# Performance work log

Hardware: AMD Instinct MI355X
Metric: run time of the kernel (lower is better)

Reference implementation:

```python
import jax, jax.numpy as jnp
import numpy as np

N = 4096
E = 262144
IN_DIM = 256
EDGE_DIM = 16
NUM_ATOM_FEATURES = 16
LATENT_DIM = 128
NUM_BOND_TYPES = 5


def setup_inputs() -> dict:
    key = jax.random.key(0)
    ks = jax.random.split(key, 12)
    inp = {
        's': jax.random.normal(ks[0], (N, IN_DIM), dtype=jnp.float32),
        'e': jax.random.normal(ks[1], (E, EDGE_DIM), dtype=jnp.float32),
        'batch': jnp.zeros((N,), dtype=jnp.int64),
        'edge_index_global': jax.random.randint(ks[2], (2, E), 0, N, dtype=jnp.int64),
        # learned parameters (torch nn.Linear layout: W is [out, in])
        'W_shared': jax.random.normal(ks[3], (IN_DIM, IN_DIM), dtype=jnp.float32) * 0.02,
        'b_shared': jnp.zeros((IN_DIM,), dtype=jnp.float32),
        'W_bond': jax.random.normal(ks[4], (IN_DIM, EDGE_DIM), dtype=jnp.float32) * 0.02,
        'b_bond': jnp.zeros((IN_DIM,), dtype=jnp.float32),
        'W_bonds': jax.random.normal(ks[5], (NUM_BOND_TYPES, IN_DIM), dtype=jnp.float32) * 0.02,
        'b_bonds': jnp.zeros((NUM_BOND_TYPES,), dtype=jnp.float32),
        'W_atoms': jax.random.normal(ks[6], (NUM_ATOM_FEATURES + LATENT_DIM, IN_DIM), dtype=jnp.float32) * 0.02,
        'b_atoms': jnp.zeros((NUM_ATOM_FEATURES + LATENT_DIM,), dtype=jnp.float32),
    }
    return inp


def reference(s, e, batch, edge_index_global,
              W_shared, b_shared, W_bond, b_bond,
              W_bonds, b_bonds, W_atoms, b_atoms):
    # shared_mapping: Linear + SiLU
    s = jax.nn.silu(s @ W_shared.T + b_shared)  # [n, in_dim]
    j = edge_index_global[0]
    i = edge_index_global[1]
    n = s.shape[0]

    # atoms_lin then split into atom-type logits and latent prediction
    atoms_out = s @ W_atoms.T + b_atoms  # [n, num_atom_features + latent_dim]
    atoms_pred = atoms_out[:, :NUM_ATOM_FEATURES]
    latent_pred = atoms_out[:, NUM_ATOM_FEATURES:]

    # dense scatter -> symmetrize -> gather (faithful to the original O(n^2) path)
    e_dense = jnp.zeros((n, n, e.shape[-1]), dtype=e.dtype).at[j, i].set(e)
    e_dense = 0.5 * (e_dense + e_dense.transpose(1, 0, 2))
    e_sym = e_dense[j, i]  # [E, edge_dim]

    # fused gather + bond linear + SiLU + bonds linear
    f = jax.nn.silu(s[i] + s[j] + e_sym @ W_bond.T + b_bond)  # [E, in_dim]
    bonds_pred = f @ W_bonds.T + b_bonds  # [E, num_bond_types]

    return (latent_pred, atoms_pred, bonds_pred)
```

## Files before the change

### kernel.cpp

```cpp
#include <hip/hip_runtime.h>
#include <hip/hip_bf16.h>

#define N_NODES   4096
#define E_EDGES   262144
#define IN_DIM    256
#define EDGE_DIM  16
#define NAF       16
#define LATENT    128
#define NBT       5

#define LATENT_OFF 0
#define ATOMS_OFF  (N_NODES * LATENT)
#define BONDS_OFF  (ATOMS_OFF + N_NODES * NAF)

#define TBITS 20
#define TSIZE (1u << TBITS)
#define TMASK (TSIZE - 1u)

typedef float    f32x4  __attribute__((ext_vector_type(4)));
typedef float    f32x4v __attribute__((ext_vector_type(4)));
typedef short    bf16x8 __attribute__((ext_vector_type(8)));
typedef unsigned u32x2  __attribute__((ext_vector_type(2)));
typedef unsigned u32x4  __attribute__((ext_vector_type(4)));

__device__ __forceinline__ float silu_f(float x) {
    return x / (1.0f + __expf(-x));
}

__device__ __forceinline__ unsigned pack_bf16x2(float lo, float hi) {
#if __has_builtin(__builtin_amdgcn_cvt_pk_bf16_f32)
    typedef __bf16 bf16x2_t __attribute__((ext_vector_type(2)));
    union { bf16x2_t v; unsigned u; } c;
    c.v = __builtin_amdgcn_cvt_pk_bf16_f32(lo, hi);
    return c.u;
#else
    union { float f; unsigned u; } a, b;
    a.f = lo; b.f = hi;
    const unsigned ra = (a.u + 0x7FFFu + ((a.u >> 16) & 1u)) >> 16;
    const unsigned rb = (b.u + 0x7FFFu + ((b.u >> 16) & 1u)) >> 16;
    return ra | (rb << 16);
#endif
}

__device__ __forceinline__ float bf_lo(unsigned u) {
    union { unsigned x; float f; } c; c.x = u << 16; return c.f;
}
__device__ __forceinline__ float bf_hi(unsigned u) {
    union { unsigned x; float f; } c; c.x = u & 0xFFFF0000u; return c.f;
}

__device__ __forceinline__ void split_bf16(const float4 x0, const float4 x1,
                                           bf16x8* hi, bf16x8* lo) {
    union { bf16x8 v; unsigned u[4]; } H, L;
    H.u[0] = pack_bf16x2(x0.x, x0.y);
    H.u[1] = pack_bf16x2(x0.z, x0.w);
    H.u[2] = pack_bf16x2(x1.x, x1.y);
    H.u[3] = pack_bf16x2(x1.z, x1.w);
    L.u[0] = pack_bf16x2(x0.x - bf_lo(H.u[0]), x0.y - bf_hi(H.u[0]));
    L.u[1] = pack_bf16x2(x0.z - bf_lo(H.u[1]), x0.w - bf_hi(H.u[1]));
    L.u[2] = pack_bf16x2(x1.x - bf_lo(H.u[2]), x1.y - bf_hi(H.u[2]));
    L.u[3] = pack_bf16x2(x1.z - bf_lo(H.u[3]), x1.w - bf_hi(H.u[3]));
    *hi = H.v; *lo = L.v;
}

__device__ __forceinline__ void gld_lds16(const void* g, void* l) {
    __builtin_amdgcn_global_load_lds(
        (const __attribute__((address_space(1))) unsigned*)g,
        (__attribute__((address_space(3))) unsigned*)l, 16, 0, 0);
}

__device__ __forceinline__ int hlookup(const unsigned long long* __restrict__ tab,
                                       unsigned key) {
    unsigned h = (key * 2654435761u) >> (32 - TBITS);
    while (true) {
        const unsigned long long cur = tab[h];
        if (cur == 0ULL) return -1;
        if ((unsigned)(cur >> 18) == key + 1u) return (int)(cur & 0x3FFFFu);
        h = (h + 1u) & TMASK;
    }
}

__global__ __launch_bounds__(256) void k_gemm1(const float* __restrict__ s,
                                               const float* __restrict__ Wsh,
                                               const float* __restrict__ bsh,
                                               const int* __restrict__ eidx,
                                               const float* __restrict__ Wb,
                                               const float* __restrict__ bb,
                                               const float* __restrict__ Wbs,
                                               unsigned short* __restrict__ sact16,
                                               unsigned long long* __restrict__ tab,
                                               u32x4* __restrict__ A1pre,
                                               u32x4* __restrict__ A2pre) {
    const int blk = blockIdx.x;
    const int c   = threadIdx.x;

    if (blk >= 1024) {
        if (blk < 2048) {
            const int k = (blk - 1024) * 256 + c;
            const unsigned j = (unsigned)eidx[k];
            const unsigned i = (unsigned)eidx[E_EDGES + k];
            const unsigned key = (j << 12) | i;
            const unsigned long long mine =
                ((unsigned long long)(key + 1u) << 18) | (unsigned)k;
            unsigned h = (key * 2654435761u) >> (32 - TBITS);
            while (true) {
                unsigned long long cur = tab[h];
                if (cur == 0ULL) {
                    const unsigned long long old = atomicCAS(&tab[h], 0ULL, mine);
                    if (old == 0ULL) return;
                    cur = old;
                }
                if ((unsigned)(cur >> 18) == key + 1u) {
                    atomicMax(&tab[h], mine);
                    return;
                }
                h = (h + 1u) & TMASK;
            }
        } else {
#pragma unroll
            for (int ee = 0; ee < 4; ++ee) {
                const int idx  = c + 256 * ee;
                const int g    = idx >> 6;
                const int lane = idx & 63;
                const int m    = lane & 15;
                const int q    = lane >> 4;

                const float4 w = *(const float4*)(Wb + (16 * g + m) * EDGE_DIM + 4 * q);
                u32x4 r1;
                r1.x = pack_bf16x2(w.x, w.y);
                r1.y = pack_bf16x2(w.z, w.w);
                r1.z = pack_bf16x2(bb[16 * g + m], 0.0f);
                r1.w = 0u;
                A1pre[idx] = r1;

                u32x4 r2;
                if (m < NBT) {
                    const float4 ws = *(const float4*)(Wbs + m * IN_DIM + 16 * g + 4 * q);
                    r2.x = pack_bf16x2(ws.x, ws.y);
                    r2.y = pack_bf16x2(ws.z, ws.w);
                } else {
                    r2.x = 0u; r2.y = 0u;
                }
                r2.z = 0u; r2.w = 0u;
                A2pre[idx] = r2;
            }
        }
        return;
    }

    const int lane = c & 63;
    const int wv   = c >> 6;
    const int wave = blk * 4 + wv;
    const int m    = lane & 15;
    const int q    = lane >> 4;
    const int row0 = (wave >> 4) * 16;
    const int col0 = (wave & 15) * 16;

    f32x4v acc;
    {
        const float bias = bsh[col0 + m];
        acc[0] = bias; acc[1] = bias; acc[2] = bias; acc[3] = bias;
    }

    const float* ap = s   + (size_t)(row0 + m) * IN_DIM + 8 * q;
    const float* bp = Wsh + (size_t)(col0 + m) * IN_DIM + 8 * q;

#pragma unroll
    for (int c8 = 0; c8 < 8; ++c8) {
        const float4 a0 = *(const float4*)(ap + 32 * c8);
        const float4 a1 = *(const float4*)(ap + 32 * c8 + 4);
        const float4 b0 = *(const float4*)(bp + 32 * c8);
        const float4 b1 = *(const float4*)(bp + 32 * c8 + 4);
        bf16x8 Ah, Al, Bh, Bl;
        split_bf16(a0, a1, &Ah, &Al);
        split_bf16(b0, b1, &Bh, &Bl);
        acc = __builtin_amdgcn_mfma_f32_16x16x32_bf16(Ah, Bh, acc, 0, 0, 0);
        acc = __builtin_amdgcn_mfma_f32_16x16x32_bf16(Al, Bh, acc, 0, 0, 0);
        acc = __builtin_amdgcn_mfma_f32_16x16x32_bf16(Ah, Bl, acc, 0, 0, 0);
    }

#pragma unroll
    for (int r = 0; r < 4; ++r) {
        const int row = row0 + 4 * q + r;
        const float v = silu_f(acc[r]);
        sact16[(size_t)row * IN_DIM + col0 + m] =
            (unsigned short)(pack_bf16x2(v, 0.0f) & 0xFFFFu);
    }
}

__global__ __launch_bounds__(256, 5) void k_edges_mfma(const int* __restrict__ eidx,
                                                       const float* __restrict__ e,
                                                       const unsigned long long* __restrict__ tab,
                                                       const unsigned short* __restrict__ sact16,
                                                       const u32x4* __restrict__ A1pre,
                                                       const u32x4* __restrict__ A2pre,
                                                       const float* __restrict__ bbs,
                                                       const float* __restrict__ Wa,
                                                       const float* __restrict__ ba,
                                                       float* __restrict__ out) {
    __shared__ unsigned lds_all[4][2048];
    const int blk  = blockIdx.x;
    const int lane = threadIdx.x & 63;
    const int wv   = threadIdx.x >> 6;
    const int m    = lane & 15;
    const int q    = lane >> 4;

    if (blk >= 4096) {
        const int wave = (blk - 4096) * 4 + wv;
        const int rt = wave / 9;
        const int ct = wave - rt * 9;
        const int row0  = rt * 16;
        const int n_abs = ct * 16 + m;

        f32x4v acc;
        {
            const float bias = ba[n_abs];
            acc[0] = bias; acc[1] = bias; acc[2] = bias; acc[3] = bias;
        }

        const unsigned short* apu = sact16 + (size_t)(row0 + m) * IN_DIM + 8 * q;
        const float*          bp  = Wa + (size_t)n_abs * IN_DIM + 8 * q;

#pragma unroll
        for (int c8 = 0; c8 < 8; ++c8) {
            const bf16x8 A = *(const bf16x8*)(apu + 32 * c8);
            const float4 b0 = *(const float4*)(bp + 32 * c8);
            const float4 b1 = *(const float4*)(bp + 32 * c8 + 4);
            bf16x8 Bh, Bl;
            split_bf16(b0, b1, &Bh, &Bl);
            acc = __builtin_amdgcn_mfma_f32_16x16x32_bf16(A, Bh, acc, 0, 0, 0);
            acc = __builtin_amdgcn_mfma_f32_16x16x32_bf16(A, Bl, acc, 0, 0, 0);
        }
#pragma unroll
        for (int r = 0; r < 4; ++r) {
            const int row = row0 + 4 * q + r;
            if (n_abs < NAF)
                out[ATOMS_OFF + (size_t)row * NAF + n_abs] = acc[r];
            else
                out[LATENT_OFF + (size_t)row * LATENT + (n_abs - NAF)] = acc[r];
        }
        return;
    }

    const int k0 = __builtin_amdgcn_readfirstlane((blk * 4 + wv) * 16);
    unsigned* myl = lds_all[wv];
    const short one_q0 = (q == 0) ? (short)0x3F80 : (short)0;

    f32x4v acc_init;
#pragma unroll
    for (int r = 0; r < 4; ++r) {
        const int bond = 4 * q + r;
        acc_init[r] = (bond < NBT) ? bbs[bond] : 0.0f;
    }

    const unsigned j_m = (unsigned)eidx[k0 + m];
    const unsigned i_m = (unsigned)eidx[E_EDGES + k0 + m];

    const char* si_base = (const char*)(sact16 + (size_t)i_m * IN_DIM);
    const char* sj_base = (const char*)(sact16 + (size_t)j_m * IN_DIM);

#pragma unroll
    for (int u = 0; u < 4; ++u)
        gld_lds16(si_base + (4 * u + q) * 16, (char*)myl + u * 1024);
#pragma unroll
    for (int u = 0; u < 4; ++u)
        gld_lds16(sj_base + (4 * u + q) * 16, (char*)myl + 4096 + u * 1024);

    const unsigned wf = (unsigned)hlookup(tab, (j_m << 12) | i_m);
    const int      wr = hlookup(tab, (i_m << 12) | j_m);

    f32x4 es = *(const f32x4*)(e + (size_t)wf * EDGE_DIM + 4 * q);
    if (wr >= 0)
        es += *(const f32x4*)(e + (size_t)wr * EDGE_DIM + 4 * q);
    es *= 0.5f;

    union { bf16x8 v; short s[8]; unsigned u[4]; } B1;
    B1.u[0] = pack_bf16x2(es[0], es[1]);
    B1.u[1] = pack_bf16x2(es[2], es[3]);
    B1.s[4] = one_q0; B1.s[5] = 0;
    B1.u[3] = 0u;

    const u32x4* a1p = A1pre + lane;
    const u32x4* a2p = A2pre + lane;

    f32x4v acc0 = acc_init;
    f32x4v acc1 = {0.0f, 0.0f, 0.0f, 0.0f};

    const int qh = q >> 1;
    const int qw = 2 * (q & 1);
    const int mw = m * 4;

    auto run_half = [&](int h) {
#pragma unroll
        for (int gp = 0; gp < 8; ++gp) {
            const int g     = 8 * h + gp;
            const int chunk = 2 * gp + qh;
            const int offw  = (chunk >> 2) * 256 + (chunk & 3) * 64 + mw + qw;

            const u32x2 wi = *(const u32x2*)(myl + offw);
            const u32x2 wj = *(const u32x2*)(myl + 1024 + offw);

            f32x4v C1;
            C1[0] = bf_lo(wi.x) + bf_lo(wj.x);
            C1[1] = bf_hi(wi.x) + bf_hi(wj.x);
            C1[2] = bf_lo(wi.y) + bf_lo(wj.y);
            C1[3] = bf_hi(wi.y) + bf_hi(wj.y);

            const u32x4 r1 = a1p[g * 64];
            const u32x4 r2 = a2p[g * 64];
            union { bf16x8 v; unsigned u[4]; } A1, A2;
            A1.u[0] = r1.x; A1.u[1] = r1.y; A1.u[2] = r1.z; A1.u[3] = 0u;
            A2.u[0] = r2.x; A2.u[1] = r2.y; A2.u[2] = 0u;   A2.u[3] = 0u;

            const f32x4v P = __builtin_amdgcn_mfma_f32_16x16x32_bf16(A1.v, B1.v, C1, 0, 0, 0);

            union { bf16x8 v; unsigned u[4]; } B2;
            B2.u[0] = pack_bf16x2(silu_f(P[0]), silu_f(P[1]));
            B2.u[1] = pack_bf16x2(silu_f(P[2]), silu_f(P[3]));
            B2.u[2] = 0u; B2.u[3] = 0u;

            if (g & 1) acc1 = __builtin_amdgcn_mfma_f32_16x16x32_bf16(A2.v, B2.v, acc1, 0, 0, 0);
            else       acc0 = __builtin_amdgcn_mfma_f32_16x16x32_bf16(A2.v, B2.v, acc0, 0, 0, 0);
        }
    };

    __asm__ __volatile__("s_waitcnt vmcnt(0)" ::: "memory");
    run_half(0);

    __asm__ __volatile__("s_waitcnt lgkmcnt(0)" ::: "memory");
#pragma unroll
    for (int u = 0; u < 4; ++u)
        gld_lds16(si_base + 256 + (4 * u + q) * 16, (char*)myl + u * 1024);
#pragma unroll
    for (int u = 0; u < 4; ++u)
        gld_lds16(sj_base + 256 + (4 * u + q) * 16, (char*)myl + 4096 + u * 1024);
    __asm__ __volatile__("s_waitcnt vmcnt(0)" ::: "memory");
    run_half(1);

    const f32x4v accT = acc0 + acc1;
    float* op = out + BONDS_OFF + (size_t)(k0 + m) * NBT;
    if (q == 0) {
        __builtin_nontemporal_store(accT[0], op + 0);
        __builtin_nontemporal_store(accT[1], op + 1);
        __builtin_nontemporal_store(accT[2], op + 2);
        __builtin_nontemporal_store(accT[3], op + 3);
    } else if (q == 1) {
        __builtin_nontemporal_store(accT[0], op + 4);
    }
}

extern "C" void kernel_launch(void* const* d_in, const int* in_sizes, int n_in,
                              void* d_out, int out_size, void* d_ws, size_t ws_size,
                              hipStream_t stream) {
    const float* s   = (const float*)d_in[0];
    const float* e   = (const float*)d_in[1];
    const int*   eix = (const int*)d_in[3];
    const float* Wsh = (const float*)d_in[4];
    const float* bsh = (const float*)d_in[5];
    const float* Wb  = (const float*)d_in[6];
    const float* bbo = (const float*)d_in[7];
    const float* Wbs = (const float*)d_in[8];
    const float* bbs = (const float*)d_in[9];
    const float* Wa  = (const float*)d_in[10];
    const float* ba  = (const float*)d_in[11];
    float* out = (float*)d_out;

    char* ws = (char*)d_ws;
    unsigned short*     sact16 = (unsigned short*)ws;
    u32x4*              A1pre  = (u32x4*)(ws + (2u << 20));
    u32x4*              A2pre  = (u32x4*)(ws + (2u << 20) + 16384);
    unsigned long long* tab    = (unsigned long long*)(ws + (3u << 20));

    (void)hipMemsetAsync(tab, 0x00, TSIZE * sizeof(unsigned long long), stream);

    k_gemm1<<<2049, 256, 0, stream>>>(s, Wsh, bsh, eix, Wb, bbo, Wbs,
                                      sact16, tab, A1pre, A2pre);
    k_edges_mfma<<<4672, 256, 0, stream>>>(eix, e, tab, sact16,
                                           A1pre, A2pre, bbs, Wa, ba, out);
}
```

Before: 194.7 us.

## Split hash build into own kernel and prefetch second half of gathers into registers

Moves the hash-table build and weight packing out of the GEMM kernel into a separate launch. In the edge kernel, the second-half node feature rows are loaded into registers early, alongside the hash lookups, and later written to LDS, instead of a second round of global-to-LDS loads issued after the first half is computed. SiLU now uses a hardware reciprocal instead of a divide. The changes aim to hide gather latency behind the first-half compute, at the cost of more registers per thread and one extra kernel launch.

Measured after the change: 231.2 us. +18.8%, slower.

```diff
diff --git a/kernel.cpp b/kernel.cpp
--- a/kernel.cpp
+++ b/kernel.cpp
@@ -24,7 +24,7 @@
 typedef unsigned u32x4  __attribute__((ext_vector_type(4)));
 
 __device__ __forceinline__ float silu_f(float x) {
-    return x / (1.0f + __expf(-x));
+    return x * __builtin_amdgcn_rcpf(1.0f + __expf(-x));
 }
 
 __device__ __forceinline__ unsigned pack_bf16x2(float lo, float hi) {
@@ -80,73 +80,74 @@
     }
 }
 
+__global__ __launch_bounds__(256) void k_hash(const int* __restrict__ eidx,
+                                              const float* __restrict__ Wb,
+                                              const float* __restrict__ bb,
+                                              const float* __restrict__ Wbs,
+                                              unsigned long long* __restrict__ tab,
+                                              u32x4* __restrict__ A1pre,
+                                              u32x4* __restrict__ A2pre) {
+    const int blk = blockIdx.x;
+    const int c   = threadIdx.x;
+
+    if (blk < 1024) {
+        const int k = blk * 256 + c;
+        const unsigned j = (unsigned)eidx[k];
+        const unsigned i = (unsigned)eidx[E_EDGES + k];
+        const unsigned key = (j << 12) | i;
+        const unsigned long long mine =
+            ((unsigned long long)(key + 1u) << 18) | (unsigned)k;
+        unsigned h = (key * 2654435761u) >> (32 - TBITS);
+        while (true) {
+            unsigned long long cur = tab[h];
+            if (cur == 0ULL) {
+                const unsigned long long old = atomicCAS(&tab[h], 0ULL, mine);
+                if (old == 0ULL) return;
+                cur = old;
+            }
+            if ((unsigned)(cur >> 18) == key + 1u) {
+                atomicMax(&tab[h], mine);
+                return;
+            }
+            h = (h + 1u) & TMASK;
+        }
+    } else {
+#pragma unroll
+        for (int ee = 0; ee < 4; ++ee) {
+            const int idx  = c + 256 * ee;
+            const int g    = idx >> 6;
+            const int lane = idx & 63;
+            const int m    = lane & 15;
+            const int q    = lane >> 4;
+
+            const float4 w = *(const float4*)(Wb + (16 * g + m) * EDGE_DIM + 4 * q);
+            u32x4 r1;
+            r1.x = pack_bf16x2(w.x, w.y);
+            r1.y = pack_bf16x2(w.z, w.w);
+            r1.z = pack_bf16x2(bb[16 * g + m], 0.0f);
+            r1.w = 0u;
+            A1pre[idx] = r1;
+
+            u32x4 r2;
+            if (m < NBT) {
+                const float4 ws = *(const float4*)(Wbs + m * IN_DIM + 16 * g + 4 * q);
+                r2.x = pack_bf16x2(ws.x, ws.y);
+                r2.y = pack_bf16x2(ws.z, ws.w);
+            } else {
+                r2.x = 0u; r2.y = 0u;
+            }
+            r2.z = 0u; r2.w = 0u;
+            A2pre[idx] = r2;
+        }
+    }
+}
+
 __global__ __launch_bounds__(256) void k_gemm1(const float* __restrict__ s,
                                                const float* __restrict__ Wsh,
                                                const float* __restrict__ bsh,
-                                               const int* __restrict__ eidx,
-                                               const float* __restrict__ Wb,
-                                               const float* __restrict__ bb,
-                                               const float* __restrict__ Wbs,
-                                               unsigned short* __restrict__ sact16,
-                                               unsigned long long* __restrict__ tab,
-                                               u32x4* __restrict__ A1pre,
-                                               u32x4* __restrict__ A2pre) {
+                                               unsigned short* __restrict__ sact16) {
     const int blk = blockIdx.x;
     const int c   = threadIdx.x;
-
-    if (blk >= 1024) {
-        if (blk < 2048) {
-            const int k = (blk - 1024) * 256 + c;
-            const unsigned j = (unsigned)eidx[k];
-            const unsigned i = (unsigned)eidx[E_EDGES + k];
-            const unsigned key = (j << 12) | i;
-            const unsigned long long mine =
-                ((unsigned long long)(key + 1u) << 18) | (unsigned)k;
-            unsigned h = (key * 2654435761u) >> (32 - TBITS);
-            while (true) {
-                unsigned long long cur = tab[h];
-                if (cur == 0ULL) {
-                    const unsigned long long old = atomicCAS(&tab[h], 0ULL, mine);
-                    if (old == 0ULL) return;
-                    cur = old;
-                }
-                if ((unsigned)(cur >> 18) == key + 1u) {
-                    atomicMax(&tab[h], mine);
-                    return;
-                }
-                h = (h + 1u) & TMASK;
-            }
-        } else {
-#pragma unroll
-            for (int ee = 0; ee < 4; ++ee) {
-                const int idx  = c + 256 * ee;
-                const int g    = idx >> 6;
-                const int lane = idx & 63;
-                const int m    = lane & 15;
-                const int q    = lane >> 4;
-
-                const float4 w = *(const float4*)(Wb + (16 * g + m) * EDGE_DIM + 4 * q);
-                u32x4 r1;
-                r1.x = pack_bf16x2(w.x, w.y);
-                r1.y = pack_bf16x2(w.z, w.w);
-                r1.z = pack_bf16x2(bb[16 * g + m], 0.0f);
-                r1.w = 0u;
-                A1pre[idx] = r1;
-
-                u32x4 r2;
-                if (m < NBT) {
-                    const float4 ws = *(const float4*)(Wbs + m * IN_DIM + 16 * g + 4 * q);
-                    r2.x = pack_bf16x2(ws.x, ws.y);
-                    r2.y = pack_bf16x2(ws.z, ws.w);
-                } else {
-                    r2.x = 0u; r2.y = 0u;
-                }
-                r2.z = 0u; r2.w = 0u;
-                A2pre[idx] = r2;
-            }
-        }
-        return;
-    }
 
     const int lane = c & 63;
     const int wv   = c >> 6;
@@ -266,6 +267,14 @@
     for (int u = 0; u < 4; ++u)
         gld_lds16(sj_base + (4 * u + q) * 16, (char*)myl + 4096 + u * 1024);
 
+    u32x4 st[8];
+#pragma unroll
+    for (int u = 0; u < 4; ++u)
+        st[u]     = *(const u32x4*)(si_base + 256 + (4 * u + q) * 16);
+#pragma unroll
+    for (int u = 0; u < 4; ++u)
+        st[4 + u] = *(const u32x4*)(sj_base + 256 + (4 * u + q) * 16);
+
     const unsigned wf = (unsigned)hlookup(tab, (j_m << 12) | i_m);
     const int      wr = hlookup(tab, (i_m << 12) | j_m);
 
@@ -328,13 +337,16 @@
     run_half(0);
 
     __asm__ __volatile__("s_waitcnt lgkmcnt(0)" ::: "memory");
-#pragma unroll
-    for (int u = 0; u < 4; ++u)
-        gld_lds16(si_base + 256 + (4 * u + q) * 16, (char*)myl + u * 1024);
-#pragma unroll
-    for (int u = 0; u < 4; ++u)
-        gld_lds16(sj_base + 256 + (4 * u + q) * 16, (char*)myl + 4096 + u * 1024);
-    __asm__ __volatile__("s_waitcnt vmcnt(0)" ::: "memory");
+    {
+        char* wp = (char*)myl + lane * 16;
+#pragma unroll
+        for (int u = 0; u < 4; ++u)
+            *((u32x4*)(wp + u * 1024)) = st[u];
+#pragma unroll
+        for (int u = 0; u < 4; ++u)
+            *((u32x4*)(wp + 4096 + u * 1024)) = st[4 + u];
+    }
+    __asm__ __volatile__("s_waitcnt lgkmcnt(0)" ::: "memory");
     run_half(1);
 
     const f32x4v accT = acc0 + acc1;
@@ -373,8 +385,8 @@
 
     (void)hipMemsetAsync(tab, 0x00, TSIZE * sizeof(unsigned long long), stream);
 
-    k_gemm1<<<2049, 256, 0, stream>>>(s, Wsh, bsh, eix, Wb, bbo, Wbs,
-                                      sact16, tab, A1pre, A2pre);
+    k_hash<<<1025, 256, 0, stream>>>(eix, Wb, bbo, Wbs, tab, A1pre, A2pre);
+    k_gemm1<<<1024, 256, 0, stream>>>(s, Wsh, bsh, sact16);
     k_edges_mfma<<<4672, 256, 0, stream>>>(eix, e, tab, sact16,
                                            A1pre, A2pre, bbs, Wa, ba, out);
 }
```

## Double-buffer node-feature staging into LDS in quarters with pipelined waits

Applied to the files above, without the earlier changes.

The edge kernel's gather of per-node activations now runs in four quarter stages over two LDS buffers. The next quarter is issued while the current one is computed, replacing two full halves separated by full vmcnt(0) stalls. Hash lookups and the edge-feature loads are issued before staging, and the reverse-edge branch becomes a branchless scaled load. SiLU uses a hardware reciprocal instead of a divide. Sched barriers pin the instruction order, and the wait counts must match the four loads per stage.

New measurement: 184.2 us. 1.06x faster.

```diff
diff --git a/kernel.cpp b/kernel.cpp
--- a/kernel.cpp
+++ b/kernel.cpp
@@ -24,7 +24,7 @@
 typedef unsigned u32x4  __attribute__((ext_vector_type(4)));
 
 __device__ __forceinline__ float silu_f(float x) {
-    return x / (1.0f + __expf(-x));
+    return x * __builtin_amdgcn_rcpf(1.0f + __expf(-x));
 }
 
 __device__ __forceinline__ unsigned pack_bf16x2(float lo, float hi) {
@@ -69,9 +69,13 @@
         (__attribute__((address_space(3))) unsigned*)l, 16, 0, 0);
 }
 
+__device__ __forceinline__ unsigned hashh(unsigned key) {
+    return (key * 2654435761u) >> (32 - TBITS);
+}
+
 __device__ __forceinline__ int hlookup(const unsigned long long* __restrict__ tab,
                                        unsigned key) {
-    unsigned h = (key * 2654435761u) >> (32 - TBITS);
+    unsigned h = hashh(key);
     while (true) {
         const unsigned long long cur = tab[h];
         if (cur == 0ULL) return -1;
@@ -80,7 +84,7 @@
     }
 }
 
-__global__ __launch_bounds__(256) void k_gemm1(const float* __restrict__ s,
+__global__ __launch_bounds__(256) void k_front(const float* __restrict__ s,
                                                const float* __restrict__ Wsh,
                                                const float* __restrict__ bsh,
                                                const int* __restrict__ eidx,
@@ -102,7 +106,7 @@
             const unsigned key = (j << 12) | i;
             const unsigned long long mine =
                 ((unsigned long long)(key + 1u) << 18) | (unsigned)k;
-            unsigned h = (key * 2654435761u) >> (32 - TBITS);
+            unsigned h = hashh(key);
             while (true) {
                 unsigned long long cur = tab[h];
                 if (cur == 0ULL) {
@@ -122,20 +126,20 @@
                 const int idx  = c + 256 * ee;
                 const int g    = idx >> 6;
                 const int lane = idx & 63;
-                const int m    = lane & 15;
-                const int q    = lane >> 4;
-
-                const float4 w = *(const float4*)(Wb + (16 * g + m) * EDGE_DIM + 4 * q);
+                const int mm   = lane & 15;
+                const int qq   = lane >> 4;
+
+                const float4 w = *(const float4*)(Wb + (16 * g + mm) * EDGE_DIM + 4 * qq);
                 u32x4 r1;
                 r1.x = pack_bf16x2(w.x, w.y);
                 r1.y = pack_bf16x2(w.z, w.w);
-                r1.z = pack_bf16x2(bb[16 * g + m], 0.0f);
+                r1.z = pack_bf16x2(bb[16 * g + mm], 0.0f);
                 r1.w = 0u;
                 A1pre[idx] = r1;
 
                 u32x4 r2;
-                if (m < NBT) {
-                    const float4 ws = *(const float4*)(Wbs + m * IN_DIM + 16 * g + 4 * q);
+                if (mm < NBT) {
+                    const float4 ws = *(const float4*)(Wbs + mm * IN_DIM + 16 * g + 4 * qq);
                     r2.x = pack_bf16x2(ws.x, ws.y);
                     r2.y = pack_bf16x2(ws.z, ws.w);
                 } else {
@@ -187,6 +191,10 @@
             (unsigned short)(pack_bf16x2(v, 0.0f) & 0xFFFFu);
     }
 }
+
+#define SB0()    __builtin_amdgcn_sched_barrier(0)
+#define LGKM0()  do { __asm__ __volatile__("s_waitcnt lgkmcnt(0)" ::: "memory"); SB0(); } while (0)
+#define VMW(n)   do { __asm__ __volatile__("s_waitcnt vmcnt(" #n ")" ::: "memory"); SB0(); } while (0)
 
 __global__ __launch_bounds__(256, 5) void k_edges_mfma(const int* __restrict__ eidx,
                                                        const float* __restrict__ e,
@@ -252,53 +260,58 @@
         const int bond = 4 * q + r;
         acc_init[r] = (bond < NBT) ? bbs[bond] : 0.0f;
     }
-
-    const unsigned j_m = (unsigned)eidx[k0 + m];
-    const unsigned i_m = (unsigned)eidx[E_EDGES + k0 + m];
-
-    const char* si_base = (const char*)(sact16 + (size_t)i_m * IN_DIM);
-    const char* sj_base = (const char*)(sact16 + (size_t)j_m * IN_DIM);
-
-#pragma unroll
-    for (int u = 0; u < 4; ++u)
-        gld_lds16(si_base + (4 * u + q) * 16, (char*)myl + u * 1024);
-#pragma unroll
-    for (int u = 0; u < 4; ++u)
-        gld_lds16(sj_base + (4 * u + q) * 16, (char*)myl + 4096 + u * 1024);
-
-    const unsigned wf = (unsigned)hlookup(tab, (j_m << 12) | i_m);
-    const int      wr = hlookup(tab, (i_m << 12) | j_m);
-
-    f32x4 es = *(const f32x4*)(e + (size_t)wf * EDGE_DIM + 4 * q);
-    if (wr >= 0)
-        es += *(const f32x4*)(e + (size_t)wr * EDGE_DIM + 4 * q);
-    es *= 0.5f;
-
-    union { bf16x8 v; short s[8]; unsigned u[4]; } B1;
-    B1.u[0] = pack_bf16x2(es[0], es[1]);
-    B1.u[1] = pack_bf16x2(es[2], es[3]);
-    B1.s[4] = one_q0; B1.s[5] = 0;
-    B1.u[3] = 0u;
-
     const u32x4* a1p = A1pre + lane;
     const u32x4* a2p = A2pre + lane;
-
-    f32x4v acc0 = acc_init;
-    f32x4v acc1 = {0.0f, 0.0f, 0.0f, 0.0f};
-
     const int qh = q >> 1;
     const int qw = 2 * (q & 1);
     const int mw = m * 4;
 
-    auto run_half = [&](int h) {
-#pragma unroll
-        for (int gp = 0; gp < 8; ++gp) {
-            const int g     = 8 * h + gp;
-            const int chunk = 2 * gp + qh;
-            const int offw  = (chunk >> 2) * 256 + (chunk & 3) * 64 + mw + qw;
-
-            const u32x2 wi = *(const u32x2*)(myl + offw);
-            const u32x2 wj = *(const u32x2*)(myl + 1024 + offw);
+    const unsigned j_m = (unsigned)eidx[k0 + m];
+    const unsigned i_m = (unsigned)eidx[E_EDGES + k0 + m];
+
+    const char* si_base = (const char*)(sact16 + (size_t)i_m * IN_DIM);
+    const char* sj_base = (const char*)(sact16 + (size_t)j_m * IN_DIM);
+
+    const int wf = hlookup(tab, (j_m << 12) | i_m);
+    const int wr = hlookup(tab, (i_m << 12) | j_m);
+
+    const float rsc = (wr >= 0) ? 0.5f : 0.0f;
+    const int   wrc = (wr >= 0) ? wr : 0;
+    const f32x4 ef = *(const f32x4*)(e + (size_t)wf  * EDGE_DIM + 4 * q);
+    const f32x4 er = *(const f32x4*)(e + (size_t)wrc * EDGE_DIM + 4 * q);
+
+    auto stage_q = [&](int p, int qb) {
+        gld_lds16(si_base + p * 128 + (q)     * 16, (char*)myl + qb);
+        gld_lds16(si_base + p * 128 + (4 + q) * 16, (char*)myl + qb + 1024);
+        gld_lds16(sj_base + p * 128 + (q)     * 16, (char*)myl + qb + 2048);
+        gld_lds16(sj_base + p * 128 + (4 + q) * 16, (char*)myl + qb + 3072);
+        SB0();
+    };
+
+    stage_q(0, 0);
+    stage_q(1, 4096);
+
+    union { bf16x8 v; short s[8]; unsigned u[4]; } B1;
+    {
+        const f32x4 es = ef * 0.5f + er * rsc;
+        B1.u[0] = pack_bf16x2(es[0], es[1]);
+        B1.u[1] = pack_bf16x2(es[2], es[3]);
+        B1.s[4] = one_q0; B1.s[5] = 0;
+        B1.u[3] = 0u;
+    }
+
+    f32x4v acc0 = acc_init;
+    f32x4v acc1 = {0.0f, 0.0f, 0.0f, 0.0f};
+
+    auto qcompute = [&](int qb4, int gbase) {
+#pragma unroll
+        for (int gp = 0; gp < 4; ++gp) {
+            const int g   = gbase + gp;
+            const int cl  = 2 * gp + qh;
+            const int off = (cl >> 2) * 256 + (cl & 3) * 64 + mw + qw;
+
+            const u32x2 wi = *(const u32x2*)(myl + qb4 + off);
+            const u32x2 wj = *(const u32x2*)(myl + qb4 + 512 + off);
 
             f32x4v C1;
             C1[0] = bf_lo(wi.x) + bf_lo(wj.x);
@@ -319,23 +332,26 @@
             B2.u[1] = pack_bf16x2(silu_f(P[2]), silu_f(P[3]));
             B2.u[2] = 0u; B2.u[3] = 0u;
 
-            if (g & 1) acc1 = __builtin_amdgcn_mfma_f32_16x16x32_bf16(A2.v, B2.v, acc1, 0, 0, 0);
-            else       acc0 = __builtin_amdgcn_mfma_f32_16x16x32_bf16(A2.v, B2.v, acc0, 0, 0, 0);
+            if (gp & 1) acc1 = __builtin_amdgcn_mfma_f32_16x16x32_bf16(A2.v, B2.v, acc1, 0, 0, 0);
+            else        acc0 = __builtin_amdgcn_mfma_f32_16x16x32_bf16(A2.v, B2.v, acc0, 0, 0, 0);
         }
     };
 
-    __asm__ __volatile__("s_waitcnt vmcnt(0)" ::: "memory");
-    run_half(0);
-
-    __asm__ __volatile__("s_waitcnt lgkmcnt(0)" ::: "memory");
-#pragma unroll
-    for (int u = 0; u < 4; ++u)
-        gld_lds16(si_base + 256 + (4 * u + q) * 16, (char*)myl + u * 1024);
-#pragma unroll
-    for (int u = 0; u < 4; ++u)
-        gld_lds16(sj_base + 256 + (4 * u + q) * 16, (char*)myl + 4096 + u * 1024);
-    __asm__ __volatile__("s_waitcnt vmcnt(0)" ::: "memory");
-    run_half(1);
+    VMW(4);
+    qcompute(0, 0);
+    LGKM0();
+    stage_q(2, 0);
+
+    VMW(4);
+    qcompute(1024, 4);
+    LGKM0();
+    stage_q(3, 4096);
+
+    VMW(4);
+    qcompute(0, 8);
+
+    VMW(0);
+    qcompute(1024, 12);
 
     const f32x4v accT = acc0 + acc1;
     float* op = out + BONDS_OFF + (size_t)(k0 + m) * NBT;
@@ -373,7 +389,7 @@
 
     (void)hipMemsetAsync(tab, 0x00, TSIZE * sizeof(unsigned long long), stream);
 
-    k_gemm1<<<2049, 256, 0, stream>>>(s, Wsh, bsh, eix, Wb, bbo, Wbs,
+    k_front<<<2049, 256, 0, stream>>>(s, Wsh, bsh, eix, Wb, bbo, Wbs,
                                       sact16, tab, A1pre, A2pre);
     k_edges_mfma<<<4672, 256, 0, stream>>>(eix, e, tab, sact16,
                                            A1pre, A2pre, bbs, Wa, ba, out);
```
